# Optimization experiments

Hardware: AMD Instinct MI355X
Metric: run time of the kernel (lower is better)

The kernel has to match this reference:

```python
import jax, jax.numpy as jnp
import numpy as np
import math

N_HEADS = 16
D_MODEL = 1024
M = D_MODEL // N_HEADS  # per-head dim = 64

def _kaiming_uniform(key, shape):
    # torch kaiming_uniform_ with a=sqrt(5) on [h, fan_in, fan_out]-style 3D tensor:
    # fan_in = shape[1] (size of dim 1), gain = sqrt(2/(1+a^2)) = sqrt(1/3)
    fan_in = shape[1]
    gain = math.sqrt(2.0 / (1.0 + 5.0))
    bound = gain * math.sqrt(3.0 / fan_in)
    return jax.random.uniform(key, shape, dtype=jnp.float32, minval=-bound, maxval=bound)

def setup_inputs() -> dict:
    key = jax.random.key(0)
    kx, kq, kk, kv, ko = jax.random.split(key, 5)
    x = jax.random.normal(kx, (4, 2048, D_MODEL), dtype=jnp.float32)
    W_q = _kaiming_uniform(kq, (N_HEADS, D_MODEL, M))
    W_k = _kaiming_uniform(kk, (N_HEADS, D_MODEL, M))
    W_v = _kaiming_uniform(kv, (N_HEADS, D_MODEL, M))
    W_o = _kaiming_uniform(ko, (N_HEADS, M, D_MODEL))
    return {"x": x, "W_q": W_q, "W_k": W_k, "W_v": W_v, "W_o": W_o}

def reference(x, W_q, W_k, W_v, W_o):
    # x: [b, s, d]; W_q/W_k/W_v: [h, d, m]; W_o: [h, m, d]
    q = jnp.einsum('bsd,hdm->bhsm', x, W_q)
    k = jnp.einsum('bsd,hdm->bhsm', x, W_k)
    v = jnp.einsum('bsd,hdm->bhsm', x, W_v)
    scale = 1.0 / math.sqrt(q.shape[-1])
    scores = jnp.einsum('bhsm,bhtm->bhst', q, k) * scale  # [b,h,s,s]
    attn = jax.nn.softmax(scores, axis=-1)
    ctx = jnp.einsum('bhst,bhtm->bhsm', attn, v)
    out = jnp.einsum('bhsm,hmd->bsd', ctx, W_o)  # sum over heads
    return out
```

## Files before the change

kernel.cpp:

```cpp
#include <hip/hip_runtime.h>
#include <hip/hip_bf16.h>

typedef __attribute__((ext_vector_type(8))) short short8;
typedef __attribute__((ext_vector_type(8))) _Float16 half8;
typedef __attribute__((ext_vector_type(4))) float f32x4;
typedef __attribute__((ext_vector_type(16))) float f32x16;
typedef __attribute__((ext_vector_type(4))) unsigned int uint4v;

#define NB 4
#define NH 16
#define NS 2048
#define ND 1024
#define NM 64
#define R_TOT 8192
#define N_QKV 3072
#define QKV_ONE 8388608
#define SCALE_Q 0.18033688011112042f

static __device__ __forceinline__ unsigned short f2h(float f) {
    _Float16 h = (_Float16)f;
    return __builtin_bit_cast(unsigned short, h);
}
static __device__ __forceinline__ unsigned cvtpk_h(float lo, float hiv) {
    unsigned r;
    asm("v_cvt_pkrtz_f16_f32 %0, %1, %2" : "=v"(r) : "v"(lo), "v"(hiv));
    return r;
}
static __device__ __forceinline__ void gl_lds16(const unsigned short* g, unsigned short* l) {
    __builtin_amdgcn_global_load_lds((const __attribute__((address_space(1))) void*)g,
                                     (__attribute__((address_space(3))) void*)l, 16, 0, 0);
}
static __device__ __forceinline__ half8 rd_swz(const unsigned short* base, int row, int col) {
    int byte = (row << 7) + (col << 1);
    byte ^= (row & 7) << 4;
    return *(const half8*)((const char*)base + byte);
}

__global__ __launch_bounds__(256) void k_convert_x(const float* __restrict__ x,
                                                   unsigned short* __restrict__ xh) {
    int i = blockIdx.x * 256 + threadIdx.x;
    const float4* xp = (const float4*)x;
    float4 v = xp[i];
    ushort4 o;
    o.x = f2h(v.x); o.y = f2h(v.y); o.z = f2h(v.z); o.w = f2h(v.w);
    ((ushort4*)xh)[i] = o;
}

__global__ __launch_bounds__(256) void k_convert_wqkv(const float* __restrict__ Wq,
                                                      const float* __restrict__ Wk,
                                                      const float* __restrict__ Wv,
                                                      unsigned short* __restrict__ BT) {
    int i = blockIdx.x * 256 + threadIdx.x;
    int d = i & 1023;
    int n = i >> 10;
    int w = n >> 10;
    int h = (n >> 6) & 15;
    int m = n & 63;
    const float* W = (w == 0) ? Wq : ((w == 1) ? Wk : Wv);
    float v = W[((size_t)h * ND + d) * NM + m];
    if (w == 0) v *= SCALE_Q;
    BT[i] = f2h(v);
}

__global__ __launch_bounds__(256) void k_convert_wo(const float* __restrict__ Wo,
                                                    unsigned short* __restrict__ BTo) {
    int i = blockIdx.x * 256 + threadIdx.x;
    int n = i & 1023;
    int d = i >> 10;
    BTo[i] = f2h(Wo[(size_t)n * ND + d]);
}

__global__ __launch_bounds__(256) void k_gemm_qkv(const unsigned short* __restrict__ A,
                                                  const unsigned short* __restrict__ BT,
                                                  unsigned short* __restrict__ qkv) {
    __shared__ unsigned short As[128 * 64];
    __shared__ unsigned short Bs[128 * 64];
    int tid = threadIdx.x;
    int bx = blockIdx.x;
    int rt = bx & 63;
    int ct = bx >> 6;
    int r0 = rt * 128, c0 = ct * 128;
    int lane = tid & 63, wid = tid >> 6;
    int l15 = lane & 15, grp = lane >> 4;
    int wr = (wid >> 1) * 64, wc = (wid & 1) * 64;

    f32x4 acc[4][4] = {};

    for (int k0 = 0; k0 < 1024; k0 += 64) {
        #pragma unroll
        for (int i = 0; i < 4; ++i) {
            int seg = wid * 4 + i;
            int row = seg * 8 + (lane >> 3);
            int sch = (lane & 7) ^ (row & 7);
            gl_lds16(A + (size_t)(r0 + row) * 1024 + k0 + sch * 8, As + seg * 512 + lane * 8);
            gl_lds16(BT + (size_t)(c0 + row) * 1024 + k0 + sch * 8, Bs + seg * 512 + lane * 8);
        }
        __syncthreads();
        #pragma unroll
        for (int ks = 0; ks < 64; ks += 32) {
            half8 af[4], bf[4];
            #pragma unroll
            for (int i = 0; i < 4; ++i)
                af[i] = rd_swz(As, wr + i * 16 + l15, ks + grp * 8);
            #pragma unroll
            for (int j = 0; j < 4; ++j)
                bf[j] = rd_swz(Bs, wc + j * 16 + l15, ks + grp * 8);
            #pragma unroll
            for (int i = 0; i < 4; ++i)
                #pragma unroll
                for (int j = 0; j < 4; ++j)
                    acc[i][j] = __builtin_amdgcn_mfma_f32_16x16x32_f16(af[i], bf[j], acc[i][j], 0, 0, 0);
        }
        __syncthreads();
    }
    #pragma unroll
    for (int j = 0; j < 4; ++j) {
        int n_base = c0 + wc + j * 16;
        int w = n_base >> 10;
        int nh = n_base + l15;
        int h = (nh >> 6) & 15;
        int m = nh & 63;
        if (w == 2) {
            unsigned short* outp = qkv + 2 * (size_t)QKV_ONE;
            #pragma unroll
            for (int i = 0; i < 4; ++i) {
                int rb = r0 + wr + i * 16 + grp * 4;
                int bb = rb >> 11, s = rb & 2047;
                ushort4 pv;
                pv.x = f2h(acc[i][j][0]);
                pv.y = f2h(acc[i][j][1]);
                pv.z = f2h(acc[i][j][2]);
                pv.w = f2h(acc[i][j][3]);
                *(ushort4*)(outp + ((size_t)(bb * NH + h) * NM + m) * NS + s) = pv;
            }
        } else {
            unsigned short* outp = qkv + (size_t)w * QKV_ONE;
            #pragma unroll
            for (int i = 0; i < 4; ++i) {
                int rb = r0 + wr + i * 16 + grp * 4;
                #pragma unroll
                for (int reg = 0; reg < 4; ++reg) {
                    int r = rb + reg;
                    int bb = r >> 11, s = r & 2047;
                    outp[((size_t)(bb * NH + h) * NS + s) * NM + m] = f2h(acc[i][j][reg]);
                }
            }
        }
    }
}

__global__ __launch_bounds__(256) void k_attn(const unsigned short* __restrict__ qkv,
                                              unsigned short* __restrict__ ctx) {
    __shared__ unsigned short Ks[2][4096];
    __shared__ unsigned short Vs[2][4096];
    __shared__ float ls[4][32];

    int tid = threadIdx.x;
    int lane = tid & 63, wid = tid >> 6;
    int l31 = lane & 31, hi = lane >> 5;

    int bid = blockIdx.x;
    int xcd = bid & 7;
    int j = bid >> 3;
    int bh = xcd * 8 + (j >> 4);
    int qb = j & 15;
    int b = bh >> 4, h = bh & 15;

    size_t hb = (size_t)bh * NS * NM;
    const unsigned short* Qg = qkv + hb;
    const unsigned short* Kg = qkv + QKV_ONE + hb;
    const unsigned short* Vt = qkv + 2 * (size_t)QKV_ONE + hb;

    int q0 = qb * 128 + wid * 32;

    half8 qf[4];
    #pragma unroll
    for (int kk = 0; kk < 4; ++kk)
        qf[kk] = *(const half8*)(Qg + (size_t)(q0 + l31) * NM + kk * 16 + hi * 8);

    f32x16 accO0 = {}, accO1 = {};
    float lsum = 0.f;

    auto stage = [&](int bufi, int t0) {
        #pragma unroll
        for (int i = 0; i < 4; ++i) {
            int seg = wid * 4 + i;
            int off = (seg & 7) * 512 + lane * 8;
            int row = off >> 6;
            int sch = ((off >> 3) & 7) ^ (row & 7);
            if (seg < 8)
                gl_lds16(Kg + (size_t)(t0 + row) * NM + sch * 8, &Ks[bufi][off]);
            else
                gl_lds16(Vt + (size_t)row * NS + t0 + sch * 8, &Vs[bufi][off]);
        }
    };

    stage(0, 0);
    __syncthreads();

    for (int t = 0; t < 32; ++t) {
        int buf = t & 1;
        if (t < 31) stage(buf ^ 1, (t + 1) * 64);
        const unsigned short* Kb = Ks[buf];
        const unsigned short* Vb = Vs[buf];

        f32x16 s0v = {}, s1v = {};
        __builtin_amdgcn_s_setprio(1);
        #pragma unroll
        for (int kk = 0; kk < 4; ++kk) {
            int col = kk * 16 + hi * 8;
            s0v = __builtin_amdgcn_mfma_f32_32x32x16_f16(rd_swz(Kb, l31, col), qf[kk], s0v, 0, 0, 0);
            s1v = __builtin_amdgcn_mfma_f32_32x32x16_f16(rd_swz(Kb, 32 + l31, col), qf[kk], s1v, 0, 0, 0);
        }
        __builtin_amdgcn_s_setprio(0);

        unsigned pk0[8], pk1[8];
        #pragma unroll
        for (int jj = 0; jj < 8; ++jj) {
            float a0 = __builtin_amdgcn_exp2f(s0v[2 * jj]);
            float b0 = __builtin_amdgcn_exp2f(s0v[2 * jj + 1]);
            float a1 = __builtin_amdgcn_exp2f(s1v[2 * jj]);
            float b1 = __builtin_amdgcn_exp2f(s1v[2 * jj + 1]);
            lsum += a0 + b0 + a1 + b1;
            pk0[jj] = cvtpk_h(a0, b0);
            pk1[jj] = cvtpk_h(a1, b1);
        }

        __builtin_amdgcn_s_setprio(1);
        #pragma unroll
        for (int kt = 0; kt < 4; ++kt) {
            unsigned w0, w1, w2, w3;
            if (kt < 2) {
                int base = (kt & 1) * 4;
                w0 = pk0[base + 0]; w1 = pk0[base + 1];
                w2 = pk0[base + 2]; w3 = pk0[base + 3];
            } else {
                int base = (kt & 1) * 4;
                w0 = pk1[base + 0]; w1 = pk1[base + 1];
                w2 = pk1[base + 2]; w3 = pk1[base + 3];
            }
            asm("v_permlane32_swap_b32 %0, %1" : "+v"(w0), "+v"(w2));
            asm("v_permlane32_swap_b32 %0, %1" : "+v"(w1), "+v"(w3));
            uint4v av;
            av[0] = w0; av[1] = w1; av[2] = w2; av[3] = w3;
            half8 af = __builtin_bit_cast(half8, av);
            int col = kt * 16 + hi * 8;
            accO0 = __builtin_amdgcn_mfma_f32_32x32x16_f16(af, rd_swz(Vb, l31, col), accO0, 0, 0, 0);
            accO1 = __builtin_amdgcn_mfma_f32_32x32x16_f16(af, rd_swz(Vb, 32 + l31, col), accO1, 0, 0, 0);
        }
        __builtin_amdgcn_s_setprio(0);
        __syncthreads();
    }

    float lt = lsum + __shfl_xor(lsum, 32);
    ls[wid][l31] = lt;
    __syncthreads();

    #pragma unroll
    for (int reg = 0; reg < 16; ++reg) {
        int q = (reg & 3) + 8 * (reg >> 2) + 4 * hi;
        float linv = 1.0f / ls[wid][q];
        size_t ob = ((size_t)b * NS + (q0 + q)) * ND + h * 64 + l31;
        ctx[ob] = f2h(accO0[reg] * linv);
        ctx[ob + 32] = f2h(accO1[reg] * linv);
    }
}

#define LDO 40
__global__ __launch_bounds__(256) void k_gemm_out(const unsigned short* __restrict__ A,
                                                  const unsigned short* __restrict__ BT,
                                                  float* __restrict__ Cf) {
    __shared__ unsigned short Ahs[128 * LDO];
    __shared__ unsigned short Bhs[128 * LDO];
    int tid = threadIdx.x;
    int bx = blockIdx.x;
    int rt = bx & 63, ct = bx >> 6;
    int r0 = rt * 128, c0 = ct * 128;
    int lane = tid & 63, wid = tid >> 6;
    int l15 = lane & 15, grp = lane >> 4;
    int wr = (wid >> 1) * 64, wc = (wid & 1) * 64;
    f32x4 acc[4][4] = {};
    int srow = tid >> 2, schunk = (tid & 3) * 8;

    for (int k0 = 0; k0 < 1024; k0 += 32) {
        __syncthreads();
        #pragma unroll
        for (int p = 0; p < 2; ++p) {
            int row = srow + p * 64;
            *(short8*)(Ahs + row * LDO + schunk) = *(const short8*)(A + (size_t)(r0 + row) * 1024 + k0 + schunk);
            *(short8*)(Bhs + row * LDO + schunk) = *(const short8*)(BT + (size_t)(c0 + row) * 1024 + k0 + schunk);
        }
        __syncthreads();
        half8 ah[4], bh[4];
        #pragma unroll
        for (int i = 0; i < 4; ++i)
            ah[i] = *(const half8*)(Ahs + (wr + i * 16 + l15) * LDO + grp * 8);
        #pragma unroll
        for (int j = 0; j < 4; ++j)
            bh[j] = *(const half8*)(Bhs + (wc + j * 16 + l15) * LDO + grp * 8);
        #pragma unroll
        for (int i = 0; i < 4; ++i)
            #pragma unroll
            for (int j = 0; j < 4; ++j)
                acc[i][j] = __builtin_amdgcn_mfma_f32_16x16x32_f16(ah[i], bh[j], acc[i][j], 0, 0, 0);
    }
    #pragma unroll
    for (int i = 0; i < 4; ++i)
        #pragma unroll
        for (int j = 0; j < 4; ++j)
            #pragma unroll
            for (int reg = 0; reg < 4; ++reg) {
                int r = r0 + wr + i * 16 + grp * 4 + reg;
                int c = c0 + wc + j * 16 + l15;
                Cf[(size_t)r * 1024 + c] = acc[i][j][reg];
            }
}

extern "C" void kernel_launch(void* const* d_in, const int* in_sizes, int n_in,
                              void* d_out, int out_size, void* d_ws, size_t ws_size,
                              hipStream_t stream) {
    (void)in_sizes; (void)n_in; (void)out_size; (void)ws_size;
    const float* x  = (const float*)d_in[0];
    const float* Wq = (const float*)d_in[1];
    const float* Wk = (const float*)d_in[2];
    const float* Wv = (const float*)d_in[3];
    const float* Wo = (const float*)d_in[4];

    char* ws = (char*)d_ws;
    unsigned short* Xh   = (unsigned short*)ws;  ws += (size_t)R_TOT * 1024 * 2;
    unsigned short* BTq  = (unsigned short*)ws;  ws += (size_t)N_QKV * 1024 * 2;
    unsigned short* BTo  = (unsigned short*)ws;  ws += (size_t)1024 * 1024 * 2;
    unsigned short* QKV  = (unsigned short*)ws;  ws += (size_t)3 * QKV_ONE * 2;
    unsigned short* Ctx  = (unsigned short*)ws;  ws += (size_t)R_TOT * 1024 * 2;

    k_convert_x<<<dim3(R_TOT * 1024 / 4 / 256), dim3(256), 0, stream>>>(x, Xh);
    k_convert_wqkv<<<dim3(N_QKV * 1024 / 256), dim3(256), 0, stream>>>(Wq, Wk, Wv, BTq);
    k_convert_wo<<<dim3(1024 * 1024 / 256), dim3(256), 0, stream>>>(Wo, BTo);
    k_gemm_qkv<<<dim3(64 * 24), dim3(256), 0, stream>>>(Xh, BTq, QKV);
    k_attn<<<dim3(1024), dim3(256), 0, stream>>>(QKV, Ctx);
    k_gemm_out<<<dim3(64 * 8), dim3(256), 0, stream>>>(Ctx, BTo, (float*)d_out);
}
```

Before: 224.2 us.

## Deepen attention K/V prefetch and use async swizzled LDS loads in output GEMM

The attention loop now keeps two tiles in flight. It issues stages for tiles t+1 and t+2 and waits with a partial vmcnt and a raw s_barrier instead of a full __syncthreads, so K/V global loads overlap more compute. The output projection GEMM switches from register-staged padded LDS copies to direct global-to-LDS loads into an XOR-swizzled 64-wide K tile, which halves the number of K iterations and barriers. The risks are correctness of the hand-tuned vmcnt counts and reduced overlap in the GEMM, which is still single-buffered.

```diff
diff --git a/kernel.cpp b/kernel.cpp
--- a/kernel.cpp
+++ b/kernel.cpp
@@ -196,11 +196,14 @@
     };
 
     stage(0, 0);
-    __syncthreads();
+    stage(1, 64);
 
     for (int t = 0; t < 32; ++t) {
         int buf = t & 1;
-        if (t < 31) stage(buf ^ 1, (t + 1) * 64);
+        if (t < 31) asm volatile("s_waitcnt vmcnt(4)" ::: "memory");
+        else        asm volatile("s_waitcnt vmcnt(0)" ::: "memory");
+        __builtin_amdgcn_s_barrier();
+        __builtin_amdgcn_sched_barrier(0);
         const unsigned short* Kb = Ks[buf];
         const unsigned short* Vb = Vs[buf];
 
@@ -249,7 +252,10 @@
             accO1 = __builtin_amdgcn_mfma_f32_32x32x16_f16(af, rd_swz(Vb, 32 + l31, col), accO1, 0, 0, 0);
         }
         __builtin_amdgcn_s_setprio(0);
-        __syncthreads();
+
+        __builtin_amdgcn_sched_barrier(0);
+        __builtin_amdgcn_s_barrier();
+        if (t < 30) stage(buf, (t + 2) * 64);
     }
 
     float lt = lsum + __shfl_xor(lsum, 32);
@@ -266,12 +272,11 @@
     }
 }
 
-#define LDO 40
 __global__ __launch_bounds__(256) void k_gemm_out(const unsigned short* __restrict__ A,
                                                   const unsigned short* __restrict__ BT,
                                                   float* __restrict__ Cf) {
-    __shared__ unsigned short Ahs[128 * LDO];
-    __shared__ unsigned short Bhs[128 * LDO];
+    __shared__ unsigned short As[128 * 64];
+    __shared__ unsigned short Bs[128 * 64];
     int tid = threadIdx.x;
     int bx = blockIdx.x;
     int rt = bx & 63, ct = bx >> 6;
@@ -280,29 +285,33 @@
     int l15 = lane & 15, grp = lane >> 4;
     int wr = (wid >> 1) * 64, wc = (wid & 1) * 64;
     f32x4 acc[4][4] = {};
-    int srow = tid >> 2, schunk = (tid & 3) * 8;
-
-    for (int k0 = 0; k0 < 1024; k0 += 32) {
+
+    for (int k0 = 0; k0 < 1024; k0 += 64) {
+        #pragma unroll
+        for (int i = 0; i < 4; ++i) {
+            int seg = wid * 4 + i;
+            int row = seg * 8 + (lane >> 3);
+            int sch = (lane & 7) ^ (row & 7);
+            gl_lds16(A + (size_t)(r0 + row) * 1024 + k0 + sch * 8, As + seg * 512 + lane * 8);
+            gl_lds16(BT + (size_t)(c0 + row) * 1024 + k0 + sch * 8, Bs + seg * 512 + lane * 8);
+        }
         __syncthreads();
         #pragma unroll
-        for (int p = 0; p < 2; ++p) {
-            int row = srow + p * 64;
-            *(short8*)(Ahs + row * LDO + schunk) = *(const short8*)(A + (size_t)(r0 + row) * 1024 + k0 + schunk);
-            *(short8*)(Bhs + row * LDO + schunk) = *(const short8*)(BT + (size_t)(c0 + row) * 1024 + k0 + schunk);
+        for (int ks = 0; ks < 64; ks += 32) {
+            half8 af[4], bf[4];
+            #pragma unroll
+            for (int i = 0; i < 4; ++i)
+                af[i] = rd_swz(As, wr + i * 16 + l15, ks + grp * 8);
+            #pragma unroll
+            for (int j = 0; j < 4; ++j)
+                bf[j] = rd_swz(Bs, wc + j * 16 + l15, ks + grp * 8);
+            #pragma unroll
+            for (int i = 0; i < 4; ++i)
+                #pragma unroll
+                for (int j = 0; j < 4; ++j)
+                    acc[i][j] = __builtin_amdgcn_mfma_f32_16x16x32_f16(af[i], bf[j], acc[i][j], 0, 0, 0);
         }
         __syncthreads();
-        half8 ah[4], bh[4];
-        #pragma unroll
-        for (int i = 0; i < 4; ++i)
-            ah[i] = *(const half8*)(Ahs + (wr + i * 16 + l15) * LDO + grp * 8);
-        #pragma unroll
-        for (int j = 0; j < 4; ++j)
-            bh[j] = *(const half8*)(Bhs + (wc + j * 16 + l15) * LDO + grp * 8);
-        #pragma unroll
-        for (int i = 0; i < 4; ++i)
-            #pragma unroll
-            for (int j = 0; j < 4; ++j)
-                acc[i][j] = __builtin_amdgcn_mfma_f32_16x16x32_f16(ah[i], bh[j], acc[i][j], 0, 0, 0);
     }
     #pragma unroll
     for (int i = 0; i < 4; ++i)
```

Result: faster. 219.6 us (-2.0%).
